# Optimization experiments

Hardware: AMD Instinct MI355X
Metric: run time of the kernel (lower is better)

Reference implementation:

```python
import jax, jax.numpy as jnp
import numpy as np

HIDDEN = 768
BATCH = 128


def setup_inputs() -> dict:
    key = jax.random.key(0)
    k_in, k_op = jax.random.split(key)
    inputs = jax.random.normal(k_in, (BATCH, HIDDEN, HIDDEN), dtype=jnp.float32)
    # nn.init.uniform_(operator, 0, 1)
    operator = jax.random.uniform(k_op, (HIDDEN, HIDDEN), dtype=jnp.float32)
    return {"inputs": inputs, "operator": operator}


def reference(inputs, operator):
    # Original: diag(operator @ inputs @ operator^T) then softmax over dim axis.
    # diag_i = sum_{j,k} operator[i,j] * inputs[b,j,k] * operator[i,k]
    # Compute first GEMM, then fuse the second matmul's diagonal as a dot-reduction.
    mm = jnp.einsum('ij,bjk->bik', operator, inputs)      # [b, d, d]
    diag = jnp.einsum('bik,ik->bi', mm, operator)          # [b, d]
    return jax.nn.softmax(diag, axis=1)
```

## Files before the change

kernel.cpp:

```cpp
#include <hip/hip_runtime.h>

#define HID 768
#define NB  128

typedef _Float16 half8   __attribute__((ext_vector_type(8)));
typedef __fp16   fp16x2  __attribute__((ext_vector_type(2)));
typedef float    float4_t __attribute__((ext_vector_type(4)));

#define OP_TILES (48 * 24)
#define OP_PLANE ((size_t)OP_TILES * 64 * 8)

__global__ __launch_bounds__(256)
void split_op(const float* __restrict__ OP, _Float16* __restrict__ ws)
{
    const int g    = blockIdx.x * 256 + threadIdx.x;
    const int tile = g >> 6, lane = g & 63;
    const int it16 = tile / 24, ks = tile % 24;
    const int i = it16 * 16 + (lane & 15);
    const int k = ks * 32 + (lane >> 4) * 8;
    const float4_t a = *(const float4_t*)(OP + (size_t)i * HID + k);
    const float4_t b = *(const float4_t*)(OP + (size_t)i * HID + k + 4);
    half8 h, l;
#pragma unroll
    for (int e = 0; e < 4; ++e) {
        _Float16 h0 = (_Float16)a[e]; h[e]     = h0; l[e]     = (_Float16)(a[e] - (float)h0);
        _Float16 h1 = (_Float16)b[e]; h[e + 4] = h1; l[e + 4] = (_Float16)(b[e] - (float)h1);
    }
    *(half8*)(ws + (size_t)(tile * 64 + lane) * 8) = h;
    *(half8*)(ws + OP_PLANE + (size_t)(tile * 64 + lane) * 8) = l;
}

__device__ __forceinline__ void convert8(const float4_t a, const float4_t b,
                                         half8& h, half8& l)
{
    fp16x2 h01 = __builtin_amdgcn_cvt_pkrtz(a[0], a[1]);
    fp16x2 h23 = __builtin_amdgcn_cvt_pkrtz(a[2], a[3]);
    fp16x2 h45 = __builtin_amdgcn_cvt_pkrtz(b[0], b[1]);
    fp16x2 h67 = __builtin_amdgcn_cvt_pkrtz(b[2], b[3]);
    fp16x2 l01 = __builtin_amdgcn_cvt_pkrtz(a[0] - (float)h01[0], a[1] - (float)h01[1]);
    fp16x2 l23 = __builtin_amdgcn_cvt_pkrtz(a[2] - (float)h23[0], a[3] - (float)h23[1]);
    fp16x2 l45 = __builtin_amdgcn_cvt_pkrtz(b[0] - (float)h45[0], b[1] - (float)h45[1]);
    fp16x2 l67 = __builtin_amdgcn_cvt_pkrtz(b[2] - (float)h67[0], b[3] - (float)h67[1]);
    h = (half8){(_Float16)h01[0], (_Float16)h01[1], (_Float16)h23[0], (_Float16)h23[1],
                (_Float16)h45[0], (_Float16)h45[1], (_Float16)h67[0], (_Float16)h67[1]};
    l = (half8){(_Float16)l01[0], (_Float16)l01[1], (_Float16)l23[0], (_Float16)l23[1],
                (_Float16)l45[0], (_Float16)l45[1], (_Float16)l67[0], (_Float16)l67[1]};
}

__global__ __launch_bounds__(256, 3)
void diag_quad_kernel(const float* __restrict__ X, const float* __restrict__ OP,
                      const _Float16* __restrict__ opws, float* __restrict__ out)
{
    __shared__ __align__(16) _Float16 Ah[4096];
    __shared__ __align__(16) _Float16 Al[4096];
    __shared__ float Dred[2][128];

    const int idx  = blockIdx.x;
    const int xcd  = idx & 7, slot = idx >> 3;
    const int b    = xcd * 16 + slot / 6;
    const int it   = slot % 6;
    const int i0   = it * 128;
    const float* Xb = X + (size_t)b * HID * HID;

    const int tid  = threadIdx.x;
    const int lane = tid & 63;
    const int wave = tid >> 6;
    const int wj   = wave & 1;
    const int wi   = wave >> 1;
    const int m16  = lane & 15;
    const int kg   = lane >> 4;

    const int row0 = tid >> 2;
    const int kgs  = tid & 3;
    const int lds0 = (row0 >> 4) * 512 + kgs * 128 + (row0 & 15) * 8;
    const int lds1 = ((row0 + 64) >> 4) * 512 + kgs * 128 + (row0 & 15) * 8;

    const int fragoff  = kg * 128 + m16 * 8;
    const int it16base = it * 8 + wi * 4;

    float p[4] = {0.f, 0.f, 0.f, 0.f};

    for (int jt = 0; jt < 6; ++jt) {
        const int j0 = jt * 128;
        float4_t acc[4][4];
#pragma unroll
        for (int a = 0; a < 4; ++a)
#pragma unroll
            for (int c = 0; c < 4; ++c) acc[a][c] = (float4_t){0.f, 0.f, 0.f, 0.f};

        for (int ks = 0; ks < 24; ++ks) {
            const int k0 = ks * 32;

            half8 bh[4], bl[4];
            const size_t obase = ((size_t)it16base * 24 + ks) * 512 + (size_t)lane * 8;
#pragma unroll
            for (int tj = 0; tj < 4; ++tj) {
                bh[tj] = *(const half8*)(opws + obase + (size_t)tj * 24 * 512);
                bl[tj] = *(const half8*)(opws + OP_PLANE + obase + (size_t)tj * 24 * 512);
            }

            const float* s0 = Xb + (size_t)(j0 + row0) * HID + k0 + kgs * 8;
            const float* s1 = Xb + (size_t)(j0 + row0 + 64) * HID + k0 + kgs * 8;
            const float4_t a0 = *(const float4_t*)(s0);
            const float4_t a1 = *(const float4_t*)(s0 + 4);
            const float4_t b0 = *(const float4_t*)(s1);
            const float4_t b1 = *(const float4_t*)(s1 + 4);
            half8 h0, l0v, h1, l1v;
            convert8(a0, a1, h0, l0v);
            convert8(b0, b1, h1, l1v);

            __syncthreads();
            *(half8*)&Ah[lds0] = h0;
            *(half8*)&Al[lds0] = l0v;
            *(half8*)&Ah[lds1] = h1;
            *(half8*)&Al[lds1] = l1v;
            __syncthreads();

#pragma unroll
            for (int ti = 0; ti < 4; ++ti) {
                const int off = (wj * 4 + ti) * 512 + fragoff;
                const half8 ah = *(const half8*)&Ah[off];
                const half8 al = *(const half8*)&Al[off];
#pragma unroll
                for (int tj = 0; tj < 4; ++tj) {
                    acc[ti][tj] = __builtin_amdgcn_mfma_f32_16x16x32_f16(ah, bh[tj], acc[ti][tj], 0, 0, 0);
                    acc[ti][tj] = __builtin_amdgcn_mfma_f32_16x16x32_f16(al, bh[tj], acc[ti][tj], 0, 0, 0);
                    acc[ti][tj] = __builtin_amdgcn_mfma_f32_16x16x32_f16(ah, bl[tj], acc[ti][tj], 0, 0, 0);
                }
            }
        }

#pragma unroll
        for (int tj = 0; tj < 4; ++tj) {
            const int i_abs = i0 + wi * 64 + tj * 16 + m16;
            float s = 0.f;
#pragma unroll
            for (int ti = 0; ti < 4; ++ti) {
                const int jb = j0 + wj * 64 + ti * 16 + kg * 4;
                const float4_t ov = *(const float4_t*)(OP + (size_t)i_abs * HID + jb);
#pragma unroll
                for (int r = 0; r < 4; ++r) s += acc[ti][tj][r] * ov[r];
            }
            p[tj] += s;
        }
    }

#pragma unroll
    for (int tj = 0; tj < 4; ++tj) {
        p[tj] += __shfl_xor(p[tj], 16);
        p[tj] += __shfl_xor(p[tj], 32);
    }
    if (kg == 0) {
#pragma unroll
        for (int tj = 0; tj < 4; ++tj)
            Dred[wj][wi * 64 + tj * 16 + m16] = p[tj];
    }
    __syncthreads();
    if (tid < 128)
        out[(size_t)b * HID + i0 + tid] = Dred[0][tid] + Dred[1][tid];
}

__global__ __launch_bounds__(768)
void softmax_rows(float* __restrict__ out)
{
    const int row = blockIdx.x;
    const int t = threadIdx.x;
    const int wave = t >> 6, lane = t & 63;
    __shared__ float redm[12];
    __shared__ float reds[12];

    float v = out[(size_t)row * HID + t];

    float m = v;
#pragma unroll
    for (int o = 32; o >= 1; o >>= 1) m = fmaxf(m, __shfl_xor(m, o));
    if (lane == 0) redm[wave] = m;
    __syncthreads();
    if (t == 0) {
        float mm = redm[0];
        for (int w = 1; w < 12; ++w) mm = fmaxf(mm, redm[w]);
        redm[0] = mm;
    }
    __syncthreads();
    m = redm[0];

    const float e = expf(v - m);
    float s = e;
#pragma unroll
    for (int o = 32; o >= 1; o >>= 1) s += __shfl_xor(s, o);
    if (lane == 0) reds[wave] = s;
    __syncthreads();
    if (t == 0) {
        float ss = 0.f;
        for (int w = 0; w < 12; ++w) ss += reds[w];
        reds[0] = ss;
    }
    __syncthreads();
    out[(size_t)row * HID + t] = e / reds[0];
}

extern "C" void kernel_launch(void* const* d_in, const int* in_sizes, int n_in,
                              void* d_out, int out_size, void* d_ws, size_t ws_size,
                              hipStream_t stream)
{
    const float* X  = (const float*)d_in[0];
    const float* OP = (const float*)d_in[1];
    float* out = (float*)d_out;
    _Float16* opws = (_Float16*)d_ws;

    hipLaunchKernelGGL(split_op, dim3(OP_TILES / 4), dim3(256), 0, stream, OP, opws);
    hipLaunchKernelGGL(diag_quad_kernel, dim3(NB * 6), dim3(256), 0, stream, X, OP, opws, out);
    hipLaunchKernelGGL(softmax_rows, dim3(NB), dim3(768), 0, stream, out);
}
```

Baseline: 635.1 us.

## Double-buffer X tiles via global_load_lds and switch to 32x32x16 MFMA

X tiles are now staged as raw fp32 into a double-buffered LDS area with async global_load_lds, so the next tile's load overlaps the current tile's compute and only one barrier is needed per step. The fp32-to-fp16 hi/lo split of X moves to after the LDS read, and the inner product uses 32x32x16 MFMA with a reworked operator workspace layout and a flattened jt/ks loop. This trades doubled LDS footprint and repeated per-wave conversion work for fewer barriers, load/compute overlap and larger MFMA tiles.

Result: slower. 769.3 us (+21.1%).

```diff
diff --git a/kernel.cpp b/kernel.cpp
--- a/kernel.cpp
+++ b/kernel.cpp
@@ -1,34 +1,16 @@
 #include <hip/hip_runtime.h>
+#include <stdint.h>
 
 #define HID 768
 #define NB  128
 
-typedef _Float16 half8   __attribute__((ext_vector_type(8)));
-typedef __fp16   fp16x2  __attribute__((ext_vector_type(2)));
+typedef _Float16 half8    __attribute__((ext_vector_type(8)));
+typedef __fp16   fp16x2   __attribute__((ext_vector_type(2)));
 typedef float    float4_t __attribute__((ext_vector_type(4)));
-
-#define OP_TILES (48 * 24)
+typedef float    f32x16   __attribute__((ext_vector_type(16)));
+
+#define OP_TILES (24 * 48)
 #define OP_PLANE ((size_t)OP_TILES * 64 * 8)
-
-__global__ __launch_bounds__(256)
-void split_op(const float* __restrict__ OP, _Float16* __restrict__ ws)
-{
-    const int g    = blockIdx.x * 256 + threadIdx.x;
-    const int tile = g >> 6, lane = g & 63;
-    const int it16 = tile / 24, ks = tile % 24;
-    const int i = it16 * 16 + (lane & 15);
-    const int k = ks * 32 + (lane >> 4) * 8;
-    const float4_t a = *(const float4_t*)(OP + (size_t)i * HID + k);
-    const float4_t b = *(const float4_t*)(OP + (size_t)i * HID + k + 4);
-    half8 h, l;
-#pragma unroll
-    for (int e = 0; e < 4; ++e) {
-        _Float16 h0 = (_Float16)a[e]; h[e]     = h0; l[e]     = (_Float16)(a[e] - (float)h0);
-        _Float16 h1 = (_Float16)b[e]; h[e + 4] = h1; l[e + 4] = (_Float16)(b[e] - (float)h1);
-    }
-    *(half8*)(ws + (size_t)(tile * 64 + lane) * 8) = h;
-    *(half8*)(ws + OP_PLANE + (size_t)(tile * 64 + lane) * 8) = l;
-}
 
 __device__ __forceinline__ void convert8(const float4_t a, const float4_t b,
                                          half8& h, half8& l)
@@ -47,12 +29,27 @@
                 (_Float16)l45[0], (_Float16)l45[1], (_Float16)l67[0], (_Float16)l67[1]};
 }
 
+__global__ __launch_bounds__(256)
+void split_op(const float* __restrict__ OP, _Float16* __restrict__ ws)
+{
+    const int g    = blockIdx.x * 256 + threadIdx.x;
+    const int tile = g >> 6, lane = g & 63;
+    const int i32t = tile / 48, k16 = tile % 48;
+    const int i = i32t * 32 + (lane & 31);
+    const int k = k16 * 16 + (lane >> 5) * 8;
+    const float4_t a = *(const float4_t*)(OP + (size_t)i * HID + k);
+    const float4_t b = *(const float4_t*)(OP + (size_t)i * HID + k + 4);
+    half8 h, l;
+    convert8(a, b, h, l);
+    *(half8*)(ws + (size_t)(tile * 64 + lane) * 8) = h;
+    *(half8*)(ws + OP_PLANE + (size_t)(tile * 64 + lane) * 8) = l;
+}
+
 __global__ __launch_bounds__(256, 3)
 void diag_quad_kernel(const float* __restrict__ X, const float* __restrict__ OP,
                       const _Float16* __restrict__ opws, float* __restrict__ out)
 {
-    __shared__ __align__(16) _Float16 Ah[4096];
-    __shared__ __align__(16) _Float16 Al[4096];
+    __shared__ __align__(16) float Abuf[2][4096];
     __shared__ float Dred[2][128];
 
     const int idx  = blockIdx.x;
@@ -67,93 +64,111 @@
     const int wave = tid >> 6;
     const int wj   = wave & 1;
     const int wi   = wave >> 1;
-    const int m16  = lane & 15;
-    const int kg   = lane >> 4;
-
-    const int row0 = tid >> 2;
-    const int kgs  = tid & 3;
-    const int lds0 = (row0 >> 4) * 512 + kgs * 128 + (row0 & 15) * 8;
-    const int lds1 = ((row0 + 64) >> 4) * 512 + kgs * 128 + (row0 & 15) * 8;
-
-    const int fragoff  = kg * 128 + m16 * 8;
-    const int it16base = it * 8 + wi * 4;
-
-    float p[4] = {0.f, 0.f, 0.f, 0.f};
-
-    for (int jt = 0; jt < 6; ++jt) {
-        const int j0 = jt * 128;
-        float4_t acc[4][4];
-#pragma unroll
-        for (int a = 0; a < 4; ++a)
-#pragma unroll
-            for (int c = 0; c < 4; ++c) acc[a][c] = (float4_t){0.f, 0.f, 0.f, 0.f};
-
-        for (int ks = 0; ks < 24; ++ks) {
-            const int k0 = ks * 32;
-
-            half8 bh[4], bl[4];
-            const size_t obase = ((size_t)it16base * 24 + ks) * 512 + (size_t)lane * 8;
-#pragma unroll
-            for (int tj = 0; tj < 4; ++tj) {
-                bh[tj] = *(const half8*)(opws + obase + (size_t)tj * 24 * 512);
-                bl[tj] = *(const half8*)(opws + OP_PLANE + obase + (size_t)tj * 24 * 512);
+    const int l5   = lane >> 5;
+    const int m32  = lane & 31;
+
+    const int srow = wave * 32 + m32;
+    const int scol = l5 * 4;
+
+    float p0 = 0.f, p1 = 0.f;
+
+#define STAGE4(bufp, srcbase)                                                          \
+    {                                                                                  \
+        const float* _s = (srcbase);                                                   \
+        _Pragma("unroll")                                                              \
+        for (int _i = 0; _i < 4; ++_i)                                                 \
+            __builtin_amdgcn_global_load_lds(                                          \
+                (const __attribute__((address_space(1))) uint32_t*)(_s + _i * 8),      \
+                (__attribute__((address_space(3))) uint32_t*)&(bufp)[(wave * 4 + _i) * 256], \
+                16, 0, 0);                                                             \
+    }
+
+    STAGE4(Abuf[0], Xb + (size_t)srow * HID + scol);
+    __syncthreads();
+
+    f32x16 acc[2][2];
+    int jt = 0, ks = 0;
+    for (int t = 0; t < 144; ++t) {
+        const int cur = t & 1;
+        const int j0  = jt * 128;
+
+        half8 bh[2][2], bl[2][2];
+#pragma unroll
+        for (int tj = 0; tj < 2; ++tj) {
+            const int i32t = it * 4 + wi * 2 + tj;
+#pragma unroll
+            for (int kh = 0; kh < 2; ++kh) {
+                const size_t o = ((size_t)(i32t * 48 + ks * 2 + kh)) * 512 + (size_t)lane * 8;
+                bh[tj][kh] = *(const half8*)(opws + o);
+                bl[tj][kh] = *(const half8*)(opws + OP_PLANE + o);
             }
-
-            const float* s0 = Xb + (size_t)(j0 + row0) * HID + k0 + kgs * 8;
-            const float* s1 = Xb + (size_t)(j0 + row0 + 64) * HID + k0 + kgs * 8;
-            const float4_t a0 = *(const float4_t*)(s0);
-            const float4_t a1 = *(const float4_t*)(s0 + 4);
-            const float4_t b0 = *(const float4_t*)(s1);
-            const float4_t b1 = *(const float4_t*)(s1 + 4);
-            half8 h0, l0v, h1, l1v;
-            convert8(a0, a1, h0, l0v);
-            convert8(b0, b1, h1, l1v);
-
-            __syncthreads();
-            *(half8*)&Ah[lds0] = h0;
-            *(half8*)&Al[lds0] = l0v;
-            *(half8*)&Ah[lds1] = h1;
-            *(half8*)&Al[lds1] = l1v;
-            __syncthreads();
-
-#pragma unroll
-            for (int ti = 0; ti < 4; ++ti) {
-                const int off = (wj * 4 + ti) * 512 + fragoff;
-                const half8 ah = *(const half8*)&Ah[off];
-                const half8 al = *(const half8*)&Al[off];
-#pragma unroll
-                for (int tj = 0; tj < 4; ++tj) {
-                    acc[ti][tj] = __builtin_amdgcn_mfma_f32_16x16x32_f16(ah, bh[tj], acc[ti][tj], 0, 0, 0);
-                    acc[ti][tj] = __builtin_amdgcn_mfma_f32_16x16x32_f16(al, bh[tj], acc[ti][tj], 0, 0, 0);
-                    acc[ti][tj] = __builtin_amdgcn_mfma_f32_16x16x32_f16(ah, bl[tj], acc[ti][tj], 0, 0, 0);
+        }
+
+        int kn = ks + 1, jn = jt;
+        if (kn == 24) { kn = 0; jn = jt + 1; }
+        if (jn < 6)
+            STAGE4(Abuf[cur ^ 1], Xb + (size_t)(jn * 128 + srow) * HID + kn * 32 + scol);
+
+        if (ks == 0) {
+#pragma unroll
+            for (int ti = 0; ti < 2; ++ti)
+#pragma unroll
+                for (int tj = 0; tj < 2; ++tj)
+#pragma unroll
+                    for (int e = 0; e < 16; ++e) acc[ti][tj][e] = 0.f;
+        }
+
+        const float* Ab = Abuf[cur];
+#pragma unroll
+        for (int ti = 0; ti < 2; ++ti) {
+            const int rt = wj * 2 + ti;
+#pragma unroll
+            for (int kh = 0; kh < 2; ++kh) {
+                const int fb = ((rt * 2 + kh) * 128 + l5 * 64 + m32) * 4;
+                const float4_t x0 = *(const float4_t*)&Ab[fb];
+                const float4_t x1 = *(const float4_t*)&Ab[fb + 128];
+                half8 ah, al;
+                convert8(x0, x1, ah, al);
+#pragma unroll
+                for (int tj = 0; tj < 2; ++tj) {
+                    acc[ti][tj] = __builtin_amdgcn_mfma_f32_32x32x16_f16(ah, bh[tj][kh], acc[ti][tj], 0, 0, 0);
+                    acc[ti][tj] = __builtin_amdgcn_mfma_f32_32x32x16_f16(al, bh[tj][kh], acc[ti][tj], 0, 0, 0);
+                    acc[ti][tj] = __builtin_amdgcn_mfma_f32_32x32x16_f16(ah, bl[tj][kh], acc[ti][tj], 0, 0, 0);
                 }
             }
         }
 
-#pragma unroll
-        for (int tj = 0; tj < 4; ++tj) {
-            const int i_abs = i0 + wi * 64 + tj * 16 + m16;
-            float s = 0.f;
-#pragma unroll
-            for (int ti = 0; ti < 4; ++ti) {
-                const int jb = j0 + wj * 64 + ti * 16 + kg * 4;
-                const float4_t ov = *(const float4_t*)(OP + (size_t)i_abs * HID + jb);
-#pragma unroll
-                for (int r = 0; r < 4; ++r) s += acc[ti][tj][r] * ov[r];
+        if (ks == 23) {
+#pragma unroll
+            for (int tj = 0; tj < 2; ++tj) {
+                const int i_abs = i0 + wi * 64 + tj * 32 + m32;
+                float s = 0.f;
+#pragma unroll
+                for (int ti = 0; ti < 2; ++ti) {
+                    const int jb = j0 + wj * 64 + ti * 32 + l5 * 4;
+#pragma unroll
+                    for (int r2 = 0; r2 < 4; ++r2) {
+                        const float4_t ov = *(const float4_t*)(OP + (size_t)i_abs * HID + jb + r2 * 8);
+                        s += acc[ti][tj][r2 * 4 + 0] * ov[0]
+                           + acc[ti][tj][r2 * 4 + 1] * ov[1]
+                           + acc[ti][tj][r2 * 4 + 2] * ov[2]
+                           + acc[ti][tj][r2 * 4 + 3] * ov[3];
+                    }
+                }
+                if (tj == 0) p0 += s; else p1 += s;
             }
-            p[tj] += s;
-        }
-    }
-
-#pragma unroll
-    for (int tj = 0; tj < 4; ++tj) {
-        p[tj] += __shfl_xor(p[tj], 16);
-        p[tj] += __shfl_xor(p[tj], 32);
-    }
-    if (kg == 0) {
-#pragma unroll
-        for (int tj = 0; tj < 4; ++tj)
-            Dred[wj][wi * 64 + tj * 16 + m16] = p[tj];
+        }
+
+        __syncthreads();
+        ks = kn; jt = jn;
+    }
+#undef STAGE4
+
+    p0 += __shfl_xor(p0, 32);
+    p1 += __shfl_xor(p1, 32);
+    if (lane < 32) {
+        Dred[wj][wi * 64 + lane]      = p0;
+        Dred[wj][wi * 64 + 32 + lane] = p1;
     }
     __syncthreads();
     if (tid < 128)
```
